# Performance work log

Measured on AMD Instinct MI355X. Metric: run time of the kernel, lower is better.

Reference implementation:

```python
import jax, jax.numpy as jnp
import numpy as np
import math

B, S, D, H = 16, 512, 1024, 16
DH = D // H  # 64
NUM_DEG = 50
NUM_SPE = 512


def setup_inputs() -> dict:
    key = jax.random.key(0)
    ks = jax.random.split(key, 16)
    w = lambda k, shape: (jax.random.normal(k, shape, jnp.float32) * 0.02)
    return {
        "hidden_states": jax.random.normal(ks[0], (B, S, D), jnp.float32),
        "attention_mask": jnp.zeros((B, 1, 1, S), jnp.float32),
        "if_2d": 1,
        "in_degree": jax.random.randint(ks[1], (B, S), 0, NUM_DEG),
        "out_degree": jax.random.randint(ks[2], (B, S), 0, NUM_DEG),
        "spe": jax.random.randint(ks[3], (B, S, S), 0, NUM_SPE),
        "dist_3d": jax.random.normal(ks[4], (B, S), jnp.float32),
        "dist_m": jax.random.normal(ks[5], (B, S, S), jnp.float32),
        # Linear params stored as [in, out]; y = x @ W + b
        "Wq": w(ks[6], (D, D)), "bq": jnp.zeros((D,), jnp.float32),
        "Wk": w(ks[7], (D, D)), "bk": jnp.zeros((D,), jnp.float32),
        "Wv": w(ks[8], (D, D)), "bv": jnp.zeros((D,), jnp.float32),
        "W_in": w(ks[9], (NUM_DEG, D)),
        "W_out": w(ks[10], (NUM_DEG, D)),
        "W_spe": w(ks[11], (NUM_SPE, H)),
    }


def reference(hidden_states, attention_mask, if_2d, in_degree, out_degree,
              spe, dist_3d, dist_m, Wq, bq, Wk, bk, Wv, bv,
              W_in, W_out, W_spe):
    # if_2d == True branch (2D graph path). padding_idx=0 -> row 0 is zero.
    pad_mask = (jnp.arange(NUM_DEG) != 0).astype(hidden_states.dtype)[:, None]
    pos = (W_in * pad_mask)[in_degree] + (W_out * pad_mask)[out_degree]  # [B,S,D]
    bias = jnp.transpose(W_spe[spe], (0, 3, 1, 2))  # [B,S,S,H] -> [B,H,S,S]

    h = hidden_states + pos
    to_heads = lambda x: x.reshape(B, S, H, DH).transpose(0, 2, 1, 3)  # [B,H,S,DH]
    q = to_heads(h @ Wq + bq)
    k = to_heads(h @ Wk + bk)
    v = to_heads(h @ Wv + bv)

    scores = jnp.einsum('bhqd,bhkd->bhqk', q, k) / math.sqrt(DH)
    scores = scores + bias + attention_mask
    probs = jax.nn.softmax(scores, axis=-1)  # dropout p=0 (eval)
    ctx = jnp.einsum('bhqk,bhkd->bhqd', probs, v)  # [B,H,S,DH]
    ctx = ctx.transpose(0, 2, 1, 3).reshape(B, S, D)
    return ctx, probs
```

## Files before the change

kernel.cpp:

```cpp
#include <hip/hip_runtime.h>

#define Bc 16
#define Sc 512
#define Dc 1024
#define Hc 16
#define DHc 64

#define AS1 __attribute__((address_space(1)))
#define AS3 __attribute__((address_space(3)))

typedef __attribute__((ext_vector_type(8))) __bf16 bf16x8;
typedef __attribute__((ext_vector_type(4))) float f32x4;
typedef __attribute__((ext_vector_type(8))) unsigned short ushort8;

static __device__ __forceinline__ unsigned short f2bf(float f) {
  unsigned int u = __builtin_bit_cast(unsigned int, f);
  unsigned int r = (u + 0x7fffu + ((u >> 16) & 1u)) >> 16;
  return (unsigned short)r;
}
static __device__ __forceinline__ float bf2f(unsigned short u) {
  unsigned int x = ((unsigned int)u) << 16;
  return __builtin_bit_cast(float, x);
}

__global__ __launch_bounds__(256) void k_prep(
    const float* __restrict__ hidden, const int* __restrict__ ind,
    const int* __restrict__ outd, const float* __restrict__ Win,
    const float* __restrict__ Wout, const float* __restrict__ Wq,
    const float* __restrict__ Wk, const float* __restrict__ Wv,
    const float* __restrict__ Wspe, const int* __restrict__ spe,
    unsigned short* __restrict__ hbf, unsigned short* __restrict__ Wtq,
    unsigned short* __restrict__ Wtk, unsigned short* __restrict__ Wtv,
    float* __restrict__ WspeT, unsigned short* __restrict__ spe16) {
  __shared__ float tile[64][65];
  int blk = blockIdx.x;
  int t = threadIdx.x;
  if (blk < 8192) {
    int row = blk;
    int id = ind[row], od = outd[row];
    float fi = (id != 0) ? 1.f : 0.f;
    float fo = (od != 0) ? 1.f : 0.f;
    float4 a = ((const float4*)(hidden + (size_t)row * Dc))[t];
    float4 x = ((const float4*)(Win + (size_t)id * Dc))[t];
    float4 y = ((const float4*)(Wout + (size_t)od * Dc))[t];
    ushort4 r;
    r.x = f2bf(a.x + fi * x.x + fo * y.x);
    r.y = f2bf(a.y + fi * x.y + fo * y.y);
    r.z = f2bf(a.z + fi * x.z + fo * y.z);
    r.w = f2bf(a.w + fi * x.w + fo * y.w);
    ((ushort4*)(hbf + (size_t)row * Dc))[t] = r;
  } else if (blk < 8960) {
    int f = blk - 8192;
    int z = f >> 8, rem = f & 255;
    int ky = rem >> 4, nx = rem & 15;
    const float* W = z == 0 ? Wq : z == 1 ? Wk : Wv;
    unsigned short* Wt = z == 0 ? Wtq : z == 1 ? Wtk : Wtv;
    int k0 = ky * 64, n0 = nx * 64;
    int r = t >> 4, c4 = (t & 15) * 4;
    for (int rr = r; rr < 64; rr += 16) {
      float4 v = *(const float4*)(W + (size_t)(k0 + rr) * Dc + n0 + c4);
      tile[rr][c4 + 0] = v.x;
      tile[rr][c4 + 1] = v.y;
      tile[rr][c4 + 2] = v.z;
      tile[rr][c4 + 3] = v.w;
    }
    __syncthreads();
    for (int rr = r; rr < 64; rr += 16) {
      ushort4 o;
      o.x = f2bf(tile[c4 + 0][rr]);
      o.y = f2bf(tile[c4 + 1][rr]);
      o.z = f2bf(tile[c4 + 2][rr]);
      o.w = f2bf(tile[c4 + 3][rr]);
      *(ushort4*)(Wt + (size_t)(n0 + rr) * Dc + k0 + c4) = o;
    }
  } else if (blk < 8992) {
    int idx = (blk - 8960) * 256 + t;
    int h = idx >> 9, i = idx & 511;
    WspeT[idx] = Wspe[i * Hc + h];
  } else {
    size_t base = (size_t)(blk - 8992) * 2048 + t * 8;
    int4 a = *(const int4*)(spe + base);
    int4 c = *(const int4*)(spe + base + 4);
    ushort8 o;
    o[0] = (unsigned short)a.x; o[1] = (unsigned short)a.y;
    o[2] = (unsigned short)a.z; o[3] = (unsigned short)a.w;
    o[4] = (unsigned short)c.x; o[5] = (unsigned short)c.y;
    o[6] = (unsigned short)c.z; o[7] = (unsigned short)c.w;
    *(ushort8*)(spe16 + base) = o;
  }
}

__global__ __launch_bounds__(256) void k_gemm_mfma(
    const unsigned short* __restrict__ hbf,
    const unsigned short* __restrict__ Wtq, const float* __restrict__ bq,
    const unsigned short* __restrict__ Wtk, const float* __restrict__ bk,
    const unsigned short* __restrict__ Wtv, const float* __restrict__ bv,
    unsigned short* __restrict__ Qo, unsigned short* __restrict__ Ko,
    unsigned short* __restrict__ Vt) {
  int zsel = blockIdx.z;
  const unsigned short* Wt;
  const float* bias;
  if (zsel == 0) { Wt = Wtq; bias = bq; }
  else if (zsel == 1) { Wt = Wtk; bias = bk; }
  else { Wt = Wtv; bias = bv; }

  __shared__ __align__(16) unsigned short As0[128 * 32];
  __shared__ __align__(16) unsigned short As1[128 * 32];
  __shared__ __align__(16) unsigned short Bs0[128 * 32];
  __shared__ __align__(16) unsigned short Bs1[128 * 32];

  int tid = threadIdx.x, lane = tid & 63, wave = tid >> 6;
  int m0 = blockIdx.y * 128, n0 = blockIdx.x * 128;
  int wr = wave >> 1, wc = wave & 1;

  f32x4 acc[4][4] = {};

  int srow = lane >> 2;
  int skb = (lane & 3) * 8;
  const unsigned short* gA = hbf + (size_t)(m0 + srow) * Dc + skb;
  const unsigned short* gB = Wt + (size_t)(n0 + srow) * Dc + skb;

  int fr = lane & 15, kg = (lane >> 4) * 8;

  for (int k0 = 0; k0 < Dc; k0 += 64) {
#pragma unroll
    for (int cc = 0; cc < 2; ++cc) {
      int c = wave + cc * 4;
      __builtin_amdgcn_global_load_lds(
          (const AS1 void*)(gA + (size_t)c * 16 * Dc + k0),
          (AS3 void*)(As0 + c * 16 * 32), 16, 0, 0);
      __builtin_amdgcn_global_load_lds(
          (const AS1 void*)(gA + (size_t)c * 16 * Dc + k0 + 32),
          (AS3 void*)(As1 + c * 16 * 32), 16, 0, 0);
      __builtin_amdgcn_global_load_lds(
          (const AS1 void*)(gB + (size_t)c * 16 * Dc + k0),
          (AS3 void*)(Bs0 + c * 16 * 32), 16, 0, 0);
      __builtin_amdgcn_global_load_lds(
          (const AS1 void*)(gB + (size_t)c * 16 * Dc + k0 + 32),
          (AS3 void*)(Bs1 + c * 16 * 32), 16, 0, 0);
    }
    __syncthreads();

    bf16x8 af[4][2], bfr[4][2];
#pragma unroll
    for (int m = 0; m < 4; ++m) {
      af[m][0] = *(const bf16x8*)(As0 + (wr * 64 + m * 16 + fr) * 32 + kg);
      af[m][1] = *(const bf16x8*)(As1 + (wr * 64 + m * 16 + fr) * 32 + kg);
    }
#pragma unroll
    for (int n = 0; n < 4; ++n) {
      bfr[n][0] = *(const bf16x8*)(Bs0 + (wc * 64 + n * 16 + fr) * 32 + kg);
      bfr[n][1] = *(const bf16x8*)(Bs1 + (wc * 64 + n * 16 + fr) * 32 + kg);
    }
#pragma unroll
    for (int m = 0; m < 4; ++m)
#pragma unroll
      for (int n = 0; n < 4; ++n) {
        acc[m][n] = __builtin_amdgcn_mfma_f32_16x16x32_bf16(af[m][0], bfr[n][0], acc[m][n], 0, 0, 0);
        acc[m][n] = __builtin_amdgcn_mfma_f32_16x16x32_bf16(af[m][1], bfr[n][1], acc[m][n], 0, 0, 0);
      }
    __syncthreads();
  }

  int fq = lane >> 4;
  if (zsel < 2) {
    unsigned short* C = (zsel == 0) ? Qo : Ko;
    float scale = (zsel == 0) ? 0.125f : 1.f;
#pragma unroll
    for (int m = 0; m < 4; ++m) {
#pragma unroll
      for (int n = 0; n < 4; ++n) {
        int col = n0 + wc * 64 + n * 16 + fr;
        float bb = bias[col];
#pragma unroll
        for (int r = 0; r < 4; ++r) {
          int row = m0 + wr * 64 + m * 16 + fq * 4 + r;
          C[(size_t)row * Dc + col] = f2bf((acc[m][n][r] + bb) * scale);
        }
      }
    }
  } else {
#pragma unroll
    for (int m = 0; m < 4; ++m) {
#pragma unroll
      for (int n = 0; n < 4; ++n) {
        int col = n0 + wc * 64 + n * 16 + fr;
        int hh = col >> 6, dh = col & 63;
        float bb = bias[col];
        int row = m0 + wr * 64 + m * 16 + fq * 4;
        int bb_ = row >> 9, ss = row & 511;
        ushort4 pk;
        pk.x = f2bf(acc[m][n][0] + bb);
        pk.y = f2bf(acc[m][n][1] + bb);
        pk.z = f2bf(acc[m][n][2] + bb);
        pk.w = f2bf(acc[m][n][3] + bb);
        *(ushort4*)(Vt + ((size_t)(bb_ * Hc + hh) * DHc + dh) * Sc + ss) = pk;
      }
    }
  }
}

#define SWB 520
__global__ __launch_bounds__(256, 8) void k_attn(
    const unsigned short* __restrict__ Qb, const unsigned short* __restrict__ Kb,
    const unsigned short* __restrict__ Vt, const unsigned short* __restrict__ spe16,
    const float* __restrict__ WspeT, const float* __restrict__ mask,
    float* __restrict__ probs, float* __restrict__ ctx) {
  extern __shared__ char smem[];
  unsigned short* S = (unsigned short*)smem;
  float* Wb = (float*)(smem + 16640);
  float* Rinv = (float*)(smem + 16640 + 2048);

  int tid = threadIdx.x, lane = tid & 63, w = tid >> 6;
  int fr = lane & 15, fq = lane >> 4, kg8 = fq * 8;

  int flat = blockIdx.x;
  int swz = (flat & 7) * 1024 + (flat >> 3);
  int h = swz & 15, qt = (swz >> 4) & 31, b = swz >> 9;
  int q0 = qt * 16;
  int rot = (flat >> 3) & 7;

  for (int i = tid; i < 512; i += 256) Wb[i] = WspeT[h * 512 + i];

  const unsigned short* spp0 =
      spe16 + (size_t)(b * Sc + q0 + w * 4) * Sc + lane * 8;
  ushort8 iv0 = *(const ushort8*)(spp0);
  ushort8 iv1 = *(const ushort8*)(spp0 + Sc);
  ushort8 iv2 = *(const ushort8*)(spp0 + 2 * Sc);
  ushort8 iv3 = *(const ushort8*)(spp0 + 3 * Sc);
  float4 mk0 = *(const float4*)(mask + b * Sc + lane * 8);
  float4 mk1 = *(const float4*)(mask + b * Sc + lane * 8 + 4);

  const unsigned short* qbase = Qb + (size_t)(b * Sc + q0) * Dc + h * DHc;
  bf16x8 af0 = *(const bf16x8*)(qbase + (size_t)fr * Dc + kg8);
  bf16x8 af1 = *(const bf16x8*)(qbase + (size_t)fr * Dc + 32 + kg8);

  const unsigned short* kptr =
      Kb + (size_t)(b * Sc + w * 16 + fr) * Dc + h * DHc;
  bf16x8 kfA0 = *(const bf16x8*)(kptr + (size_t)rot * 64 * Dc + kg8);
  bf16x8 kfA1 = *(const bf16x8*)(kptr + (size_t)rot * 64 * Dc + 32 + kg8);
#pragma unroll
  for (int i = 0; i < 8; ++i) {
    int it = (i + rot) & 7;
    bf16x8 kfB0, kfB1;
    if (i < 7) {
      int itn = (i + 1 + rot) & 7;
      const unsigned short* np = kptr + (size_t)itn * 64 * Dc;
      kfB0 = *(const bf16x8*)(np + kg8);
      kfB1 = *(const bf16x8*)(np + 32 + kg8);
    }
    f32x4 acc = {};
    __builtin_amdgcn_s_setprio(1);
    acc = __builtin_amdgcn_mfma_f32_16x16x32_bf16(kfA0, af0, acc, 0, 0, 0);
    acc = __builtin_amdgcn_mfma_f32_16x16x32_bf16(kfA1, af1, acc, 0, 0, 0);
    __builtin_amdgcn_s_setprio(0);
    ushort4 pk;
    pk.x = f2bf(acc[0]); pk.y = f2bf(acc[1]);
    pk.z = f2bf(acc[2]); pk.w = f2bf(acc[3]);
    *(ushort4*)(S + fr * SWB + it * 64 + w * 16 + fq * 4) = pk;
    kfA0 = kfB0; kfA1 = kfB1;
  }
  __syncthreads();

  float ri0, ri1, ri2, ri3;
  {
#pragma unroll
    for (int r4 = 0; r4 < 4; ++r4) {
      int row = w * 4 + r4;
      ushort8 iv = (r4 == 0) ? iv0 : (r4 == 1) ? iv1 : (r4 == 2) ? iv2 : iv3;
      ushort8 sv = *(const ushort8*)(S + row * SWB + lane * 8);
      float e0 = __expf(bf2f(sv[0]) + Wb[iv[0]] + mk0.x);
      float e1 = __expf(bf2f(sv[1]) + Wb[iv[1]] + mk0.y);
      float e2 = __expf(bf2f(sv[2]) + Wb[iv[2]] + mk0.z);
      float e3 = __expf(bf2f(sv[3]) + Wb[iv[3]] + mk0.w);
      float e4 = __expf(bf2f(sv[4]) + Wb[iv[4]] + mk1.x);
      float e5 = __expf(bf2f(sv[5]) + Wb[iv[5]] + mk1.y);
      float e6 = __expf(bf2f(sv[6]) + Wb[iv[6]] + mk1.z);
      float e7 = __expf(bf2f(sv[7]) + Wb[iv[7]] + mk1.w);
      float sum = e0 + e1 + e2 + e3 + e4 + e5 + e6 + e7;
#pragma unroll
      for (int o = 32; o; o >>= 1) sum += __shfl_xor(sum, o);
      float rinv = 1.f / sum;
      if (r4 == 0) ri0 = rinv;
      else if (r4 == 1) ri1 = rinv;
      else if (r4 == 2) ri2 = rinv;
      else ri3 = rinv;
      ushort8 ev;
      ev[0] = f2bf(e0); ev[1] = f2bf(e1); ev[2] = f2bf(e2); ev[3] = f2bf(e3);
      ev[4] = f2bf(e4); ev[5] = f2bf(e5); ev[6] = f2bf(e6); ev[7] = f2bf(e7);
      *(ushort8*)(S + row * SWB + lane * 8) = ev;
      if (lane == 0) Rinv[row] = rinv;
    }
  }
  __syncthreads();

  const unsigned short* vptr =
      Vt + ((size_t)(b * Hc + h) * DHc + w * 16 + fr) * Sc;
  float* pbase = probs + (size_t)((b * Hc + h) * Sc + q0) * Sc;
  int prow = tid >> 4, pc0 = (tid & 15) * 4;
  float prv = (fq == 0) ? ri0 : (fq == 1) ? ri1 : (fq == 2) ? ri2 : ri3;
  f32x4 pacc0 = {}, pacc1 = {};
  bf16x8 vfA0 = *(const bf16x8*)(vptr + rot * 64 + kg8);
  bf16x8 vfA1 = *(const bf16x8*)(vptr + rot * 64 + 32 + kg8);
  ushort4 svA = *(const ushort4*)(S + prow * SWB + rot * 64 + pc0);
#pragma unroll
  for (int i = 0; i < 8; ++i) {
    int it = (i + rot) & 7;
    bf16x8 vfB0, vfB1;
    ushort4 svB;
    if (i < 7) {
      int itn = (i + 1 + rot) & 7;
      vfB0 = *(const bf16x8*)(vptr + itn * 64 + kg8);
      vfB1 = *(const bf16x8*)(vptr + itn * 64 + 32 + kg8);
      svB = *(const ushort4*)(S + prow * SWB + itn * 64 + pc0);
    }
    {
      f32x4 e;
      e[0] = bf2f(svA.x) * prv; e[1] = bf2f(svA.y) * prv;
      e[2] = bf2f(svA.z) * prv; e[3] = bf2f(svA.w) * prv;
      __builtin_nontemporal_store(e, (f32x4*)(pbase + (size_t)prow * Sc + it * 64 + pc0));
    }
    bf16x8 pfr0 = *(const bf16x8*)(S + fr * SWB + it * 64 + kg8);
    bf16x8 pfr1 = *(const bf16x8*)(S + fr * SWB + it * 64 + 32 + kg8);
    __builtin_amdgcn_s_setprio(1);
    pacc0 = __builtin_amdgcn_mfma_f32_16x16x32_bf16(vfA0, pfr0, pacc0, 0, 0, 0);
    pacc1 = __builtin_amdgcn_mfma_f32_16x16x32_bf16(vfA1, pfr1, pacc1, 0, 0, 0);
    __builtin_amdgcn_s_setprio(0);
    vfA0 = vfB0; vfA1 = vfB1; svA = svB;
  }

  {
    float rv = Rinv[fr];
    f32x4 o;
    o[0] = (pacc0[0] + pacc1[0]) * rv;
    o[1] = (pacc0[1] + pacc1[1]) * rv;
    o[2] = (pacc0[2] + pacc1[2]) * rv;
    o[3] = (pacc0[3] + pacc1[3]) * rv;
    __builtin_nontemporal_store(
        o, (f32x4*)(ctx + (size_t)(b * Sc + q0 + fr) * Dc + h * DHc + w * 16 + fq * 4));
  }
}

extern "C" void kernel_launch(void* const* d_in, const int* in_sizes, int n_in,
                              void* d_out, int out_size, void* d_ws, size_t ws_size,
                              hipStream_t stream) {
  const float* hidden = (const float*)d_in[0];
  const float* amask = (const float*)d_in[1];
  const int* ind = (const int*)d_in[3];
  const int* outd = (const int*)d_in[4];
  const int* spe = (const int*)d_in[5];
  const float* Wq = (const float*)d_in[8];
  const float* bq = (const float*)d_in[9];
  const float* Wk = (const float*)d_in[10];
  const float* bk = (const float*)d_in[11];
  const float* Wv = (const float*)d_in[12];
  const float* bv = (const float*)d_in[13];
  const float* Win = (const float*)d_in[14];
  const float* Wout = (const float*)d_in[15];
  const float* Wspe = (const float*)d_in[16];

  char* ws = (char*)d_ws;
  const size_t BSD = (size_t)Bc * Sc * Dc;
  unsigned short* hbf = (unsigned short*)ws;
  unsigned short* Wtq = (unsigned short*)(ws + 16u * 1048576);
  unsigned short* Wtk = (unsigned short*)(ws + 18u * 1048576);
  unsigned short* Wtv = (unsigned short*)(ws + 20u * 1048576);
  float* WspeT = (float*)(ws + 22u * 1048576);
  unsigned short* Qb = (unsigned short*)(ws + 24u * 1048576);
  unsigned short* Kb = (unsigned short*)(ws + 40u * 1048576);
  unsigned short* Vt = (unsigned short*)(ws + 56u * 1048576);
  unsigned short* spe16 = (unsigned short*)(ws + 72u * 1048576);
  float* ctx = (float*)d_out;
  float* probs = (float*)d_out + BSD;

  (void)hipFuncSetAttribute((const void*)k_attn,
                            hipFuncAttributeMaxDynamicSharedMemorySize, 18752);

  k_prep<<<dim3(11040), 256, 0, stream>>>(hidden, ind, outd, Win, Wout, Wq, Wk,
                                          Wv, Wspe, spe, hbf, Wtq, Wtk, Wtv,
                                          WspeT, spe16);
  k_gemm_mfma<<<dim3(8, 64, 3), 256, 0, stream>>>(hbf, Wtq, bq, Wtk, bk, Wtv, bv, Qb, Kb, Vt);
  k_attn<<<dim3(8192), 256, 18752, stream>>>(Qb, Kb, Vt, spe16, WspeT, amask, probs, ctx);
}
```

Measured before the change: 228.7 us.

## Double-buffer LDS tiles in QKV GEMM to prefetch next K-slice during MFMA

The QKV projection GEMM loop now works in K-steps of 32 over two ping-pong LDS buffers. It issues the global-to-LDS loads for the next slice before running the MFMAs on the current one, so memory latency can overlap with compute instead of sitting behind a barrier. The cost is twice as many iterations and barriers per tile. The async LDS DMA still has to complete by each barrier, which caps how much overlap is possible.

New measurement: 245.7 us. 1.07x slower.

```diff
diff --git a/kernel.cpp b/kernel.cpp
--- a/kernel.cpp
+++ b/kernel.cpp
@@ -104,10 +104,8 @@
   else if (zsel == 1) { Wt = Wtk; bias = bk; }
   else { Wt = Wtv; bias = bv; }
 
-  __shared__ __align__(16) unsigned short As0[128 * 32];
-  __shared__ __align__(16) unsigned short As1[128 * 32];
-  __shared__ __align__(16) unsigned short Bs0[128 * 32];
-  __shared__ __align__(16) unsigned short Bs1[128 * 32];
+  __shared__ __align__(16) unsigned short As[2][128 * 32];
+  __shared__ __align__(16) unsigned short Bs[2][128 * 32];
 
   int tid = threadIdx.x, lane = tid & 63, wave = tid >> 6;
   int m0 = blockIdx.y * 128, n0 = blockIdx.x * 128;
@@ -122,45 +120,40 @@
 
   int fr = lane & 15, kg = (lane >> 4) * 8;
 
-  for (int k0 = 0; k0 < Dc; k0 += 64) {
-#pragma unroll
-    for (int cc = 0; cc < 2; ++cc) {
-      int c = wave + cc * 4;
-      __builtin_amdgcn_global_load_lds(
-          (const AS1 void*)(gA + (size_t)c * 16 * Dc + k0),
-          (AS3 void*)(As0 + c * 16 * 32), 16, 0, 0);
-      __builtin_amdgcn_global_load_lds(
-          (const AS1 void*)(gA + (size_t)c * 16 * Dc + k0 + 32),
-          (AS3 void*)(As1 + c * 16 * 32), 16, 0, 0);
-      __builtin_amdgcn_global_load_lds(
-          (const AS1 void*)(gB + (size_t)c * 16 * Dc + k0),
-          (AS3 void*)(Bs0 + c * 16 * 32), 16, 0, 0);
-      __builtin_amdgcn_global_load_lds(
-          (const AS1 void*)(gB + (size_t)c * 16 * Dc + k0 + 32),
-          (AS3 void*)(Bs1 + c * 16 * 32), 16, 0, 0);
-    }
+#define STAGE(buf, k0)                                                        \
+  {                                                                           \
+    _Pragma("unroll") for (int cc = 0; cc < 2; ++cc) {                        \
+      int c = wave + cc * 4;                                                  \
+      __builtin_amdgcn_global_load_lds(                                       \
+          (const AS1 void*)(gA + (size_t)c * 16 * Dc + (k0)),                 \
+          (AS3 void*)(As[buf] + c * 16 * 32), 16, 0, 0);                      \
+      __builtin_amdgcn_global_load_lds(                                       \
+          (const AS1 void*)(gB + (size_t)c * 16 * Dc + (k0)),                 \
+          (AS3 void*)(Bs[buf] + c * 16 * 32), 16, 0, 0);                      \
+    }                                                                         \
+  }
+
+  STAGE(0, 0);
+  __syncthreads();
+
+  for (int t = 0; t < 32; ++t) {
+    int cur = t & 1;
+    if (t < 31) STAGE(cur ^ 1, (t + 1) * 32);
+    bf16x8 af[4], bfr[4];
+#pragma unroll
+    for (int m = 0; m < 4; ++m)
+      af[m] = *(const bf16x8*)(As[cur] + (wr * 64 + m * 16 + fr) * 32 + kg);
+#pragma unroll
+    for (int n = 0; n < 4; ++n)
+      bfr[n] = *(const bf16x8*)(Bs[cur] + (wc * 64 + n * 16 + fr) * 32 + kg);
+#pragma unroll
+    for (int m = 0; m < 4; ++m)
+#pragma unroll
+      for (int n = 0; n < 4; ++n)
+        acc[m][n] = __builtin_amdgcn_mfma_f32_16x16x32_bf16(af[m], bfr[n], acc[m][n], 0, 0, 0);
     __syncthreads();
-
-    bf16x8 af[4][2], bfr[4][2];
-#pragma unroll
-    for (int m = 0; m < 4; ++m) {
-      af[m][0] = *(const bf16x8*)(As0 + (wr * 64 + m * 16 + fr) * 32 + kg);
-      af[m][1] = *(const bf16x8*)(As1 + (wr * 64 + m * 16 + fr) * 32 + kg);
-    }
-#pragma unroll
-    for (int n = 0; n < 4; ++n) {
-      bfr[n][0] = *(const bf16x8*)(Bs0 + (wc * 64 + n * 16 + fr) * 32 + kg);
-      bfr[n][1] = *(const bf16x8*)(Bs1 + (wc * 64 + n * 16 + fr) * 32 + kg);
-    }
-#pragma unroll
-    for (int m = 0; m < 4; ++m)
-#pragma unroll
-      for (int n = 0; n < 4; ++n) {
-        acc[m][n] = __builtin_amdgcn_mfma_f32_16x16x32_bf16(af[m][0], bfr[n][0], acc[m][n], 0, 0, 0);
-        acc[m][n] = __builtin_amdgcn_mfma_f32_16x16x32_bf16(af[m][1], bfr[n][1], acc[m][n], 0, 0, 0);
-      }
-    __syncthreads();
-  }
+  }
+#undef STAGE
 
   int fq = lane >> 4;
   if (zsel < 2) {
```
